# Optimization experiments

Measured on AMD Instinct MI355X. Metric: run time of the kernel, lower is better.

The kernel has to match this reference:

```python
import jax, jax.numpy as jnp
import numpy as np

D_HIDDEN = 512
N_HEADS = 8
D_HEAD = D_HIDDEN // N_HEADS
LAYER_IDX = 0
FACTOR = 0.5 / float(np.sqrt(D_HEAD))


def setup_inputs() -> dict:
    key = jax.random.key(0)
    ks = jax.random.split(key, 16)
    B, N, d = 4, 2048, D_HIDDEN
    s = 1.0 / float(np.sqrt(d))
    inp = {
        "H": jax.random.normal(ks[0], (B, N, d), jnp.float32),
        "V": jax.random.normal(ks[1], (B, N, 3, d), jnp.float32),
        "D": jax.random.normal(ks[2], (B, N, N), jnp.float32),
        "rbf": jax.random.normal(ks[3], (1, B, 1, N, N), jnp.float32),
        "mask": jnp.ones((B, N), jnp.int32),
        # learned parameters (torch nn.Linear: y = x @ W.T + b)
        "Wq": jax.random.normal(ks[4], (4 * d, d), jnp.float32) * s,
        "bq": jax.random.normal(ks[5], (4 * d,), jnp.float32) * s,
        "Wk": jax.random.normal(ks[6], (4 * d, d), jnp.float32) * s,
        "bk": jax.random.normal(ks[7], (4 * d,), jnp.float32) * s,
        "Wv": jax.random.normal(ks[8], (d, d), jnp.float32) * s,
        "bv": jax.random.normal(ks[9], (d,), jnp.float32) * s,
        "Wvv": jax.random.normal(ks[10], (d, d), jnp.float32) * s,
        "Wo": jax.random.normal(ks[11], (d, d), jnp.float32) * s,
        "bo": jax.random.normal(ks[12], (d,), jnp.float32) * s,
        "Wvo": jax.random.normal(ks[13], (d, d), jnp.float32) * s,
    }
    return inp


def reference(H, V, D, rbf, mask, Wq, bq, Wk, bk, Wv, bv, Wvv, Wo, bo, Wvo):
    B, N, d = H.shape
    nh, dh = N_HEADS, D_HEAD
    # projections
    Hq = (H @ Wq.T + bq).reshape(B, N, nh, 4 * dh)
    Hk = (H @ Wk.T + bk).reshape(B, N, nh, 4 * dh)
    Hv = (H @ Wv.T + bv).reshape(B, N, nh, dh)
    # vector values: [B,N,3,nh,dh] -> [B,N,nh,3,dh] -> [B,N,nh,3*dh]
    Vv = (V @ Wvv.T).reshape(B, N, 3, nh, dh)
    Vv = jnp.swapaxes(Vv, -2, -3).reshape(B, N, nh, 3 * dh)
    V_attn = jnp.concatenate([Hv, Vv], axis=-1)  # [B,N,nh,4*dh]
    # additive geometric bias + key mask
    bias = rbf[LAYER_IDX] + D[:, None]  # [B,1,N,N]
    bias = jnp.where(mask[:, None, None, :] == 0, -jnp.inf, bias)
    # attention
    scores = jnp.einsum('bnhd,bmhd->bhnm', Hq, Hk) * FACTOR + bias
    attn = jax.nn.softmax(scores, axis=-1)
    res = jnp.einsum('bhnm,bmhd->bnhd', attn, V_attn)  # [B,N,nh,4*dh]
    # split scalar / vector outputs
    H_res = res[..., :dh].reshape(B, N, d)
    V_res = res[..., dh:].reshape(B, N, nh, 3, dh)
    V_res = jnp.swapaxes(V_res, -2, -3).reshape(B, N, 3, d)
    H_o = H_res @ Wo.T + bo
    V_o = V_res @ Wvo.T
    return H_o, V_o
```

## Files before the change

kernel.cpp:

```cpp
#include <hip/hip_runtime.h>
#include <hip/hip_bf16.h>
#include <stdint.h>

typedef __hip_bfloat16 bf16;
typedef __attribute__((ext_vector_type(8))) short bf16x8;
typedef __attribute__((ext_vector_type(4))) float f32x4;
typedef __attribute__((ext_vector_type(16))) float f32x16;
typedef __attribute__((ext_vector_type(4))) unsigned short u16x4;

#define DEVI __device__ __forceinline__

static constexpr float LOG2E = 1.44269504088896f;
static constexpr float FACTOR_L2E = 0.0625f * 1.44269504088896f;

DEVI unsigned short bfbits(float x) {
  return __builtin_bit_cast(unsigned short, __float2bfloat16(x));
}
DEVI float b2f(unsigned short u) {
  return __builtin_bit_cast(float, (uint32_t)u << 16);
}

__global__ void cvt_plain(const float* __restrict__ src, bf16* __restrict__ dst, int n) {
  int i = (blockIdx.x * 256 + threadIdx.x) * 4;
  if (i >= n) return;
  float4 v = *reinterpret_cast<const float4*>(src + i);
  union { unsigned short u[4]; uint64_t d; } t;
  t.u[0] = bfbits(v.x); t.u[1] = bfbits(v.y); t.u[2] = bfbits(v.z); t.u[3] = bfbits(v.w);
  *reinterpret_cast<uint64_t*>(dst + i) = t.d;
}

__global__ void cvt_vperm(const float* __restrict__ src, bf16* __restrict__ dst) {
  int g = blockIdx.x * 256 + threadIdx.x;
  int k4  = (g & 127) * 4;
  int rem = g >> 7;
  int c  = rem % 3;
  int bn = rem / 3;
  float4 v = *reinterpret_cast<const float4*>(src + (size_t)rem * 512 + k4);
  union { unsigned short u[4]; uint64_t d; } t;
  t.u[0] = bfbits(v.x); t.u[1] = bfbits(v.y); t.u[2] = bfbits(v.z); t.u[3] = bfbits(v.w);
  *reinterpret_cast<uint64_t*>(dst + ((size_t)c * 8192 + bn) * 512 + k4) = t.d;
}

__global__ void cvt_weights(const float* __restrict__ wq, const float* __restrict__ wk,
                            const float* __restrict__ wv, const float* __restrict__ wvv,
                            const float* __restrict__ wo, const float* __restrict__ wvo,
                            bf16* __restrict__ dst) {
  int blk = blockIdx.x;
  const float* s; int off;
  if      (blk < 1024) { s = wq  + blk * 1024;          off = 0       + blk * 1024; }
  else if (blk < 2048) { s = wk  + (blk - 1024) * 1024; off = 1048576 + (blk - 1024) * 1024; }
  else if (blk < 2304) { s = wv  + (blk - 2048) * 1024; off = 2097152 + (blk - 2048) * 1024; }
  else if (blk < 2560) { s = wvv + (blk - 2304) * 1024; off = 2359296 + (blk - 2304) * 1024; }
  else if (blk < 2816) { s = wo  + (blk - 2560) * 1024; off = 2621440 + (blk - 2560) * 1024; }
  else                 { s = wvo + (blk - 2816) * 1024; off = 2883584 + (blk - 2816) * 1024; }
  int i = threadIdx.x * 4;
  float4 v = *reinterpret_cast<const float4*>(s + i);
  union { unsigned short u[4]; uint64_t d; } t;
  t.u[0] = bfbits(v.x); t.u[1] = bfbits(v.y); t.u[2] = bfbits(v.z); t.u[3] = bfbits(v.w);
  *reinterpret_cast<uint64_t*>(dst + off + i) = t.d;
}

__global__ void bias_combine(const float* __restrict__ D, const float* __restrict__ rbf,
                             const int* __restrict__ mask, bf16* __restrict__ Bc) {
  size_t i = ((size_t)blockIdx.x * 256 + threadIdx.x) * 4;
  int col = (int)(i & 2047);
  int b   = (int)(i >> 22);
  float4 d = *reinterpret_cast<const float4*>(D + i);
  float4 r = *reinterpret_cast<const float4*>(rbf + i);
  const int* mrow = mask + b * 2048 + col;
  union { unsigned short u[4]; uint64_t dd; } t;
  t.u[0] = mrow[0] ? bfbits((d.x + r.x) * LOG2E) : bfbits(-1e30f);
  t.u[1] = mrow[1] ? bfbits((d.y + r.y) * LOG2E) : bfbits(-1e30f);
  t.u[2] = mrow[2] ? bfbits((d.z + r.z) * LOG2E) : bfbits(-1e30f);
  t.u[3] = mrow[3] ? bfbits((d.w + r.w) * LOG2E) : bfbits(-1e30f);
  *reinterpret_cast<uint64_t*>(Bc + i) = t.dd;
}

template<int MODE>
__global__ __launch_bounds__(256, 2) void gemm2(const bf16* __restrict__ A,
                                                const bf16* __restrict__ W,
                                                const bf16* __restrict__ W2,
                                                const float* __restrict__ bias,
                                                const float* __restrict__ bias2,
                                                void* __restrict__ outp) {
  constexpr int K = 512;
  __shared__ bf16 As[2][4096];
  __shared__ bf16 Bs[2][4096];
  const int tid = threadIdx.x;
  const int wid = tid >> 6, lane = tid & 63;
  const int lr = lane & 15, lg = lane >> 4;
  const int wr = wid >> 1, wc = wid & 1;
  const int bm = blockIdx.y * 128, bn = blockIdx.x * 128;

  const bf16* Wp;
  if constexpr (MODE == 0) Wp = W;
  else Wp = (blockIdx.y < 64) ? W : W2;

  const int q  = tid >> 2;
  const int ch = ((tid & 3) ^ ((tid >> 3) & 3)) * 8;
  const bf16* Asrc0 = A  + (size_t)(bm + q) * K + ch;
  const bf16* Asrc1 = A  + (size_t)(bm + 64 + q) * K + ch;
  const bf16* Wsrc0 = Wp + (size_t)(bn + q) * K + ch;
  const bf16* Wsrc1 = Wp + (size_t)(bn + 64 + q) * K + ch;
  const int wofs = wid * 1024;

  f32x4 acc[4][4];
#pragma unroll
  for (int m = 0; m < 4; m++)
#pragma unroll
    for (int n = 0; n < 4; n++) acc[m][n] = (f32x4){0.f, 0.f, 0.f, 0.f};

  __builtin_amdgcn_global_load_lds((const char*)Asrc0, (char*)&As[0][0] + wofs,        16, 0, 0);
  __builtin_amdgcn_global_load_lds((const char*)Asrc1, (char*)&As[0][0] + 4096 + wofs, 16, 0, 0);
  __builtin_amdgcn_global_load_lds((const char*)Wsrc0, (char*)&Bs[0][0] + wofs,        16, 0, 0);
  __builtin_amdgcn_global_load_lds((const char*)Wsrc1, (char*)&Bs[0][0] + 4096 + wofs, 16, 0, 0);
  __syncthreads();

  const int fxor = ((lr >> 1) & 3) << 4;
  for (int kt = 0; kt < 16; ++kt) {
    const int cur = kt & 1;
    if (kt < 15) {
      const int nxt = cur ^ 1;
      __builtin_amdgcn_global_load_lds((const char*)(Asrc0 + (kt + 1) * 32), (char*)&As[nxt][0] + wofs,        16, 0, 0);
      __builtin_amdgcn_global_load_lds((const char*)(Asrc1 + (kt + 1) * 32), (char*)&As[nxt][0] + 4096 + wofs, 16, 0, 0);
      __builtin_amdgcn_global_load_lds((const char*)(Wsrc0 + (kt + 1) * 32), (char*)&Bs[nxt][0] + wofs,        16, 0, 0);
      __builtin_amdgcn_global_load_lds((const char*)(Wsrc1 + (kt + 1) * 32), (char*)&Bs[nxt][0] + 4096 + wofs, 16, 0, 0);
    }
    const char* AsC = (const char*)&As[cur][0];
    const char* BsC = (const char*)&Bs[cur][0];
    bf16x8 af[4], bfr[4];
#pragma unroll
    for (int m = 0; m < 4; m++) {
      const int row = wr * 64 + m * 16 + lr;
      af[m] = *reinterpret_cast<const bf16x8*>(AsC + row * 64 + ((lg << 4) ^ fxor));
    }
#pragma unroll
    for (int n = 0; n < 4; n++) {
      const int row = wc * 64 + n * 16 + lr;
      bfr[n] = *reinterpret_cast<const bf16x8*>(BsC + row * 64 + ((lg << 4) ^ fxor));
    }
#pragma unroll
    for (int m = 0; m < 4; m++)
#pragma unroll
      for (int n = 0; n < 4; n++)
        acc[m][n] = __builtin_amdgcn_mfma_f32_16x16x32_bf16(af[m], bfr[n], acc[m][n], 0, 0, 0);
    __syncthreads();
  }

#pragma unroll
  for (int m = 0; m < 4; m++) {
#pragma unroll
    for (int n = 0; n < 4; n++) {
      const int col  = bn + wc * 64 + n * 16 + lr;
      const int row0 = bm + wr * 64 + m * 16 + lg * 4;
      if constexpr (MODE == 0) {
        const int isK = col >> 11;
        const int col2 = col & 2047;
        const float bb = isK ? bias2[col2] : bias[col2];
        const int hh = col2 >> 8, t = col2 & 255;
        bf16* out = (bf16*)outp + (size_t)isK * 16777216;
#pragma unroll
        for (int qq = 0; qq < 4; qq++) {
          const int row = row0 + qq;
          const int b = row >> 11, nn = row & 2047;
          float v = acc[m][n][qq] + bb;
          if (!isK) v *= FACTOR_L2E;
          out[(size_t)((b * 8 + hh) * 2048 + nn) * 256 + t] = __float2bfloat16(v);
        }
      } else if constexpr (MODE == 1) {
        bf16* out = (bf16*)outp;
        const int hh = col >> 6, t = col & 63;
        int dimrow, nn; float bb;
        if (row0 < 8192) {
          const int b = row0 >> 11; nn = row0 & 2047;
          dimrow = (b * 8 + hh) * 256 + t;
          bb = bias[col];
        } else {
          const int r = row0 - 8192;
          const int c = r >> 13, b = (r >> 11) & 3; nn = r & 2047;
          dimrow = (b * 8 + hh) * 256 + 64 + c * 64 + t;
          bb = 0.f;
        }
        const int i4 = (nn >> 2) & 7;
        const int o4 = (i4 & 4) | ((i4 & 1) << 1) | ((i4 >> 1) & 1);
        const int nn2 = (nn & ~31) | (o4 << 2);
        union { unsigned short u[4]; uint64_t d; } pk;
#pragma unroll
        for (int qq = 0; qq < 4; qq++) pk.u[qq] = bfbits(acc[m][n][qq] + bb);
        *reinterpret_cast<uint64_t*>(out + (size_t)dimrow * 2048 + nn2) = pk.d;
      } else {
        float* out = (float*)outp;
        if (row0 < 8192) {
          const float bb = bias[col];
#pragma unroll
          for (int qq = 0; qq < 4; qq++)
            out[(size_t)(row0 + qq) * 512 + col] = acc[m][n][qq] + bb;
        } else {
#pragma unroll
          for (int qq = 0; qq < 4; qq++)
            out[4194304 + (size_t)(row0 - 8192 + qq) * 512 + col] = acc[m][n][qq];
        }
      }
    }
  }
}

__global__ __launch_bounds__(256, 2) void attn_kernel(
    const bf16* __restrict__ Qg, const bf16* __restrict__ Kg, const bf16* __restrict__ Vtg,
    const bf16* __restrict__ Bc, bf16* __restrict__ Hres, bf16* __restrict__ Vres) {
  __shared__ bf16 Ks[2][32 * 256];
  __shared__ bf16 Vs[2][256 * 32];

  const int g = blockIdx.x;
  const int x = g & 7, loc = g >> 3;
  const int bh = x * 4 + (loc & 3);
  const int qt = loc >> 2;
  const int b = bh >> 3, h = bh & 7;
  const int tid = threadIdx.x, w = tid >> 6, lane = tid & 63;
  const int lq = lane & 31, hi = lane >> 5;
  const int q0 = qt * 128 + w * 32;

  const bf16* Qb = Qg + (size_t)bh * 2048 * 256;
  const char* KbC = (const char*)(Kg + (size_t)bh * 2048 * 256);
  const char* VbC = (const char*)(Vtg + (size_t)bh * 256 * 2048);
  const bf16* Bb = Bc + ((size_t)(b * 2048 + q0 + lq)) * 2048 + hi * 4;

  bf16x8 qf[16];
#pragma unroll
  for (int kc = 0; kc < 16; kc++)
    qf[kc] = *reinterpret_cast<const bf16x8*>(Qb + (size_t)(q0 + lq) * 256 + kc * 16 + hi * 8);

  f32x16 O[8];
#pragma unroll
  for (int dt = 0; dt < 8; dt++)
#pragma unroll
    for (int r = 0; r < 16; r++) O[dt][r] = 0.f;
  float mrun = -INFINITY, lrun = 0.f;

  const char* ksrc[4]; const char* vsrc[4];
#pragma unroll
  for (int i = 0; i < 4; i++) {
    const int krow = w * 8 + 2 * i + hi;
    ksrc[i] = KbC + (size_t)krow * 512 + ((lq * 16) ^ ((krow & 31) << 4));
    const int vrow = w * 64 + i * 16 + (lane >> 2);
    const int gg = ((vrow >> 1) ^ (vrow >> 3)) & 3;
    vsrc[i] = VbC + (size_t)vrow * 4096 + (((lane & 3) ^ gg) << 4);
  }

  {
    char* dK = (char*)&Ks[0][0] + w * 4096;
    char* dV = (char*)&Vs[0][0] + w * 4096;
#pragma unroll
    for (int i = 0; i < 4; i++) {
      __builtin_amdgcn_global_load_lds(ksrc[i], dK + i * 1024, 16, 0, 0);
      __builtin_amdgcn_global_load_lds(vsrc[i], dV + i * 1024, 16, 0, 0);
    }
  }
  asm volatile("s_waitcnt vmcnt(0)" ::: "memory");
  __builtin_amdgcn_sched_barrier(0);
  __builtin_amdgcn_s_barrier();

  for (int kt = 0; kt < 64; ++kt) {
    const int cur = kt & 1;
    u16x4 bg[4];
#pragma unroll
    for (int i = 0; i < 4; i++)
      bg[i] = *reinterpret_cast<const u16x4*>(Bb + kt * 32 + i * 8);
    if (kt < 63) {
      char* dK = (char*)&Ks[cur ^ 1][0] + w * 4096;
      char* dV = (char*)&Vs[cur ^ 1][0] + w * 4096;
#pragma unroll
      for (int i = 0; i < 4; i++) {
        __builtin_amdgcn_global_load_lds(ksrc[i] + (size_t)(kt + 1) * 16384, dK + i * 1024, 16, 0, 0);
        __builtin_amdgcn_global_load_lds(vsrc[i] + (size_t)(kt + 1) * 64,    dV + i * 1024, 16, 0, 0);
      }
    }
    __builtin_amdgcn_sched_barrier(0);

    const char* KsC = (const char*)&Ks[cur][0];
    f32x16 s;
#pragma unroll
    for (int r = 0; r < 16; r++) s[r] = 0.f;
    const int kxor = lq << 4;
#pragma unroll
    for (int kc = 0; kc < 16; kc++) {
      bf16x8 kf = *reinterpret_cast<const bf16x8*>(KsC + lq * 512 + ((kc * 32 + hi * 16) ^ kxor));
      s = __builtin_amdgcn_mfma_f32_32x32x16_bf16(kf, qf[kc], s, 0, 0, 0);
    }
#pragma unroll
    for (int r = 0; r < 16; r++)
      s[r] += b2f((unsigned short)bg[r >> 2][r & 3]);

    float m0 = fmaxf(s[0], s[1]),  m1 = fmaxf(s[2], s[3]);
    float m2 = fmaxf(s[4], s[5]),  m3 = fmaxf(s[6], s[7]);
    float m4 = fmaxf(s[8], s[9]),  m5 = fmaxf(s[10], s[11]);
    float m6 = fmaxf(s[12], s[13]), m7 = fmaxf(s[14], s[15]);
    float pmax = fmaxf(fmaxf(fmaxf(m0, m1), fmaxf(m2, m3)),
                       fmaxf(fmaxf(m4, m5), fmaxf(m6, m7)));
    pmax = fmaxf(pmax, __shfl_xor(pmax, 32));

    const bool ok = (pmax <= mrun + 8.f);
    if (!__all((int)ok)) {
      const float mnew = fmaxf(mrun, pmax);
      const float scq = exp2f(mrun - mnew);
      mrun = mnew;
      lrun *= scq;
      float sfac[16];
#pragma unroll
      for (int r = 0; r < 16; r++) sfac[r] = __shfl(scq, (r & 3) + 8 * (r >> 2) + 4 * hi);
#pragma unroll
      for (int dt = 0; dt < 8; dt++)
#pragma unroll
        for (int r = 0; r < 16; r++) O[dt][r] *= sfac[r];
    }

    union { unsigned short u[8]; bf16x8 v; } pa0, pa1;
    float rs = 0.f;
#pragma unroll
    for (int j = 0; j < 8; j++) {
      const float p = exp2f(s[j] - mrun);
      pa0.u[j] = bfbits(p);
      rs += b2f(pa0.u[j]);
    }
#pragma unroll
    for (int j = 0; j < 8; j++) {
      const float p = exp2f(s[8 + j] - mrun);
      pa1.u[j] = bfbits(p);
      rs += b2f(pa1.u[j]);
    }
    rs += __shfl_xor(rs, 32);
    lrun += rs;

    const char* VsC = (const char*)&Vs[cur][0];
#pragma unroll
    for (int dt = 0; dt < 8; dt++) {
      const int row = dt * 32 + lq;
      const int gg = ((row >> 1) ^ (row >> 3)) & 3;
      bf16x8 v0 = *reinterpret_cast<const bf16x8*>(VsC + row * 64 + ((hi ^ gg) << 4));
      bf16x8 v1 = *reinterpret_cast<const bf16x8*>(VsC + row * 64 + (((2 + hi) ^ gg) << 4));
      O[dt] = __builtin_amdgcn_mfma_f32_32x32x16_bf16(pa0.v, v0, O[dt], 0, 0, 0);
      O[dt] = __builtin_amdgcn_mfma_f32_32x32x16_bf16(pa1.v, v1, O[dt], 0, 0, 0);
    }

    if (kt < 63) {
      asm volatile("s_waitcnt vmcnt(0)" ::: "memory");
      __builtin_amdgcn_sched_barrier(0);
      __builtin_amdgcn_s_barrier();
    }
  }

  const float rli = 1.0f / lrun;
  float rl[16];
#pragma unroll
  for (int r = 0; r < 16; r++) rl[r] = __shfl(rli, (r & 3) + 8 * (r >> 2) + 4 * hi);
#pragma unroll
  for (int dt = 0; dt < 8; dt++) {
    const int d = dt * 32 + lq;
#pragma unroll
    for (int r = 0; r < 16; r++) {
      const int row = q0 + (r & 3) + 8 * (r >> 2) + 4 * hi;
      const float v = O[dt][r] * rl[r];
      if (d < 64) {
        Hres[(size_t)(b * 2048 + row) * 512 + h * 64 + d] = __float2bfloat16(v);
      } else {
        const int c = (d - 64) >> 6, t = (d - 64) & 63;
        Vres[((size_t)(b * 2048 + row) * 3 + c) * 512 + h * 64 + t] = __float2bfloat16(v);
      }
    }
  }
}

extern "C" void kernel_launch(void* const* d_in, const int* in_sizes, int n_in,
                              void* d_out, int out_size, void* d_ws, size_t ws_size,
                              hipStream_t stream) {
  const float* H   = (const float*)d_in[0];
  const float* V   = (const float*)d_in[1];
  const float* Dm  = (const float*)d_in[2];
  const float* rbf = (const float*)d_in[3];
  const int*   mask= (const int*)d_in[4];
  const float* Wq  = (const float*)d_in[5];
  const float* bq  = (const float*)d_in[6];
  const float* Wk  = (const float*)d_in[7];
  const float* bk  = (const float*)d_in[8];
  const float* Wv  = (const float*)d_in[9];
  const float* bv  = (const float*)d_in[10];
  const float* Wvv = (const float*)d_in[11];
  const float* Wo  = (const float*)d_in[12];
  const float* bo  = (const float*)d_in[13];
  const float* Wvo = (const float*)d_in[14];

  char* ws = (char*)d_ws;
  bf16* Hbf  = (bf16*)(ws);
  bf16* Wall = (bf16*)(ws + 33554432);
  bf16* Qw   = (bf16*)(ws + 39845888);
  bf16* Kw   = Qw + 16777216;
  bf16* Vtw  = (bf16*)(ws + 106954752);
  bf16* Hres = Hbf;
  bf16* Wqb  = Wall;
  bf16* Wvb  = Wall + 2097152;
  bf16* Wvvb = Wall + 2359296;
  bf16* Wob  = Wall + 2621440;
  bf16* Wvob = Wall + 2883584;
  bf16* Bcb  = (bf16*)d_out;

  bias_combine<<<16384, 256, 0, stream>>>(Dm, rbf, mask, Bcb);
  cvt_plain<<<4096, 256, 0, stream>>>(H, Hbf, 4194304);
  cvt_vperm<<<12288, 256, 0, stream>>>(V, Hbf + 4194304);
  cvt_weights<<<3072, 256, 0, stream>>>(Wq, Wk, Wv, Wvv, Wo, Wvo, Wall);

  gemm2<0><<<dim3(32, 64), 256, 0, stream>>>(Hbf, Wqb, nullptr, bq, bk, Qw);
  gemm2<1><<<dim3(4, 256), 256, 0, stream>>>(Hbf, Wvb, Wvvb, bv, nullptr, Vtw);

  attn_kernel<<<512, 256, 0, stream>>>(Qw, Kw, Vtw, Bcb, Hres, Hbf + 4194304);

  gemm2<2><<<dim3(4, 256), 256, 0, stream>>>(Hbf, Wob, Wvob, bo, nullptr, d_out);
}
```

Before: 441.8 us.

## Use 8-wave attention blocks with triple-buffered K/V and deeper prefetch

The attention kernel now runs 512-thread blocks that each cover 256 queries, so one block per CU shares every K/V tile across 8 waves instead of two 4-wave blocks each loading their own copy. K/V staging moves from double to triple buffering and prefetches two tiles ahead. The bias tile is prefetched one iteration early, and the loop waits only partially on the memory counter instead of draining all loads before each barrier. The goal is to cut redundant global-to-LDS traffic and hide load latency behind the MFMA work. The cost is more LDS per block, heavier barriers across 8 waves, and fragile hand-counted vmcnt values.

```diff
diff --git a/kernel.cpp b/kernel.cpp
--- a/kernel.cpp
+++ b/kernel.cpp
@@ -205,11 +205,11 @@
   }
 }
 
-__global__ __launch_bounds__(256, 2) void attn_kernel(
+__global__ __launch_bounds__(512, 1) void attn_kernel(
     const bf16* __restrict__ Qg, const bf16* __restrict__ Kg, const bf16* __restrict__ Vtg,
     const bf16* __restrict__ Bc, bf16* __restrict__ Hres, bf16* __restrict__ Vres) {
-  __shared__ bf16 Ks[2][32 * 256];
-  __shared__ bf16 Vs[2][256 * 32];
+  __shared__ bf16 Ks[3][32 * 256];
+  __shared__ bf16 Vs[3][256 * 32];
 
   const int g = blockIdx.x;
   const int x = g & 7, loc = g >> 3;
@@ -218,7 +218,7 @@
   const int b = bh >> 3, h = bh & 7;
   const int tid = threadIdx.x, w = tid >> 6, lane = tid & 63;
   const int lq = lane & 31, hi = lane >> 5;
-  const int q0 = qt * 128 + w * 32;
+  const int q0 = qt * 256 + w * 32;
 
   const bf16* Qb = Qg + (size_t)bh * 2048 * 256;
   const char* KbC = (const char*)(Kg + (size_t)bh * 2048 * 256);
@@ -237,47 +237,63 @@
     for (int r = 0; r < 16; r++) O[dt][r] = 0.f;
   float mrun = -INFINITY, lrun = 0.f;
 
-  const char* ksrc[4]; const char* vsrc[4];
-#pragma unroll
-  for (int i = 0; i < 4; i++) {
-    const int krow = w * 8 + 2 * i + hi;
-    ksrc[i] = KbC + (size_t)krow * 512 + ((lq * 16) ^ ((krow & 31) << 4));
-    const int vrow = w * 64 + i * 16 + (lane >> 2);
+  const char* ksrc[2]; const char* vsrc[2];
+#pragma unroll
+  for (int i = 0; i < 2; i++) {
+    const int X = w * 2048 + i * 1024 + lane * 16;
+    const int krow = X >> 9, kcol = X & 511;
+    ksrc[i] = KbC + (size_t)krow * 512 + (kcol ^ ((krow & 31) << 4));
+    const int vrow = X >> 6;
     const int gg = ((vrow >> 1) ^ (vrow >> 3)) & 3;
     vsrc[i] = VbC + (size_t)vrow * 4096 + (((lane & 3) ^ gg) << 4);
   }
-
-  {
-    char* dK = (char*)&Ks[0][0] + w * 4096;
-    char* dV = (char*)&Vs[0][0] + w * 4096;
-#pragma unroll
-    for (int i = 0; i < 4; i++) {
-      __builtin_amdgcn_global_load_lds(ksrc[i], dK + i * 1024, 16, 0, 0);
-      __builtin_amdgcn_global_load_lds(vsrc[i], dV + i * 1024, 16, 0, 0);
-    }
-  }
-  asm volatile("s_waitcnt vmcnt(0)" ::: "memory");
+  char* ldsKw = (char*)Ks + w * 2048;
+  char* ldsVw = (char*)Vs + w * 2048;
+
+  u16x4 bg[4];
+#pragma unroll
+  for (int i = 0; i < 4; i++) bg[i] = *reinterpret_cast<const u16x4*>(Bb + i * 8);
+  __builtin_amdgcn_sched_barrier(0);
+#pragma unroll
+  for (int i = 0; i < 2; i++) {
+    __builtin_amdgcn_global_load_lds(ksrc[i], ldsKw + i * 1024, 16, 0, 0);
+    __builtin_amdgcn_global_load_lds(vsrc[i], ldsVw + i * 1024, 16, 0, 0);
+  }
+  __builtin_amdgcn_sched_barrier(0);
+#pragma unroll
+  for (int i = 0; i < 2; i++) {
+    __builtin_amdgcn_global_load_lds(ksrc[i] + 16384, ldsKw + 16384 + i * 1024, 16, 0, 0);
+    __builtin_amdgcn_global_load_lds(vsrc[i] + 64,    ldsVw + 16384 + i * 1024, 16, 0, 0);
+  }
+  __builtin_amdgcn_sched_barrier(0);
+  asm volatile("s_waitcnt vmcnt(4)" ::: "memory");
   __builtin_amdgcn_sched_barrier(0);
   __builtin_amdgcn_s_barrier();
 
+  int c0 = 0;
+  int cs = 2;
+
+#pragma unroll 1
   for (int kt = 0; kt < 64; ++kt) {
-    const int cur = kt & 1;
-    u16x4 bg[4];
+    const int bt1 = (kt < 63) ? kt + 1 : 63;
+    u16x4 bgn[4];
 #pragma unroll
     for (int i = 0; i < 4; i++)
-      bg[i] = *reinterpret_cast<const u16x4*>(Bb + kt * 32 + i * 8);
-    if (kt < 63) {
-      char* dK = (char*)&Ks[cur ^ 1][0] + w * 4096;
-      char* dV = (char*)&Vs[cur ^ 1][0] + w * 4096;
-#pragma unroll
-      for (int i = 0; i < 4; i++) {
-        __builtin_amdgcn_global_load_lds(ksrc[i] + (size_t)(kt + 1) * 16384, dK + i * 1024, 16, 0, 0);
-        __builtin_amdgcn_global_load_lds(vsrc[i] + (size_t)(kt + 1) * 64,    dV + i * 1024, 16, 0, 0);
+      bgn[i] = *reinterpret_cast<const u16x4*>(Bb + bt1 * 32 + i * 8);
+    __builtin_amdgcn_sched_barrier(0);
+    {
+      const int st2 = (kt < 62) ? kt + 2 : 63;
+      char* dK = ldsKw + cs * 16384;
+      char* dV = ldsVw + cs * 16384;
+#pragma unroll
+      for (int i = 0; i < 2; i++) {
+        __builtin_amdgcn_global_load_lds(ksrc[i] + (size_t)st2 * 16384, dK + i * 1024, 16, 0, 0);
+        __builtin_amdgcn_global_load_lds(vsrc[i] + (size_t)st2 * 64,    dV + i * 1024, 16, 0, 0);
       }
     }
     __builtin_amdgcn_sched_barrier(0);
 
-    const char* KsC = (const char*)&Ks[cur][0];
+    const char* KsC = (const char*)Ks + c0 * 16384;
     f32x16 s;
 #pragma unroll
     for (int r = 0; r < 16; r++) s[r] = 0.f;
@@ -331,7 +347,7 @@
     rs += __shfl_xor(rs, 32);
     lrun += rs;
 
-    const char* VsC = (const char*)&Vs[cur][0];
+    const char* VsC = (const char*)Vs + c0 * 16384;
 #pragma unroll
     for (int dt = 0; dt < 8; dt++) {
       const int row = dt * 32 + lq;
@@ -342,11 +358,14 @@
       O[dt] = __builtin_amdgcn_mfma_f32_32x32x16_bf16(pa1.v, v1, O[dt], 0, 0, 0);
     }
 
-    if (kt < 63) {
-      asm volatile("s_waitcnt vmcnt(0)" ::: "memory");
-      __builtin_amdgcn_sched_barrier(0);
-      __builtin_amdgcn_s_barrier();
-    }
+    asm volatile("s_waitcnt vmcnt(5)" ::: "memory");
+    __builtin_amdgcn_sched_barrier(0);
+    __builtin_amdgcn_s_barrier();
+
+    c0 = (c0 == 2) ? 0 : c0 + 1;
+    cs = (cs == 2) ? 0 : cs + 1;
+#pragma unroll
+    for (int i = 0; i < 4; i++) bg[i] = bgn[i];
   }
 
   const float rli = 1.0f / lrun;
@@ -411,7 +430,7 @@
   gemm2<0><<<dim3(32, 64), 256, 0, stream>>>(Hbf, Wqb, nullptr, bq, bk, Qw);
   gemm2<1><<<dim3(4, 256), 256, 0, stream>>>(Hbf, Wvb, Wvvb, bv, nullptr, Vtw);
 
-  attn_kernel<<<512, 256, 0, stream>>>(Qw, Kw, Vtw, Bcb, Hres, Hbf + 4194304);
+  attn_kernel<<<256, 512, 0, stream>>>(Qw, Kw, Vtw, Bcb, Hres, Hbf + 4194304);
 
   gemm2<2><<<dim3(4, 256), 256, 0, stream>>>(Hbf, Wob, Wvob, bo, nullptr, d_out);
 }
```

Result: slower. 451.7 us (+2.2%).
